# Optimization experiments

Measured on AMD Instinct MI355X. Metric: run time of the kernel, lower is better.

Reference implementation:

```python
import jax, jax.numpy as jnp
import numpy as np
import math

DIM = 1024
NUM_HEADS = 16


def setup_inputs() -> dict:
    key = jax.random.key(0)
    ks = jax.random.split(key, 6)
    B, S, D = 2, 2048, DIM
    return {
        "q": jax.random.normal(ks[0], (B, S, D), dtype=jnp.float32),
        "k": jax.random.normal(ks[1], (B, S, D), dtype=jnp.float32),
        "v": jax.random.normal(ks[2], (B, S, D), dtype=jnp.float32),
        "wq": jax.random.normal(ks[3], (D, D), dtype=jnp.float32),
        "wk": jax.random.normal(ks[4], (D, D), dtype=jnp.float32),
        "wv": jax.random.normal(ks[5], (D, D), dtype=jnp.float32),
    }


def reference(q, k, v, wq, wk, wv):
    B, S, D = q.shape
    H = NUM_HEADS
    hd = D // H
    # projections: [B,S,D] @ [D,D]
    qp = (q @ wq).reshape(B, H, S, hd)  # NOTE: direct reshape, as in the original
    kp = (k @ wk).reshape(B, H, S, hd)
    vp = (v @ wv).reshape(B, H, S, hd)
    scale = 1.0 / math.sqrt(D)  # original scales by sqrt(dim), not sqrt(head_dim)
    att = jnp.einsum("bhqd,bhkd->bhqk", qp, kp) * scale  # [B,H,S,S]
    att = jax.nn.softmax(att, axis=-1)
    out = jnp.einsum("bhqk,bhkd->bhqd", att, vp)  # [B,H,S,hd]
    out = out.transpose(0, 2, 1, 3).reshape(B, S, D)
    return out
```

## Files before the change

### kernel.cpp

```cpp
#include <hip/hip_runtime.h>
#include <hip/hip_bf16.h>
#include <stdint.h>

#define DIMD 1024
#define SEQ  2048
#define NH   16
#define MROWS 4096
#define NQ   65536

typedef __bf16 bf16_t;
typedef bf16_t bf16x8 __attribute__((ext_vector_type(8)));
typedef float  f32x4  __attribute__((ext_vector_type(4)));
typedef unsigned short u16;
typedef unsigned short u16x4 __attribute__((ext_vector_type(4)));
typedef unsigned short u16x8 __attribute__((ext_vector_type(8)));
typedef unsigned int   u32;
typedef u32 u32x2 __attribute__((ext_vector_type(2)));

static __device__ __forceinline__ f32x4 mfma16(bf16x8 a, bf16x8 b, f32x4 c) {
    return __builtin_amdgcn_mfma_f32_16x16x32_bf16(a, b, c, 0, 0, 0);
}

static __device__ __forceinline__ float fast_exp2(float x) {
#if __has_builtin(__builtin_amdgcn_exp2f)
    return __builtin_amdgcn_exp2f(x);
#else
    return exp2f(x);
#endif
}

#define GLD16(gsrc, ldst) __builtin_amdgcn_global_load_lds(                    \
    (const __attribute__((address_space(1))) unsigned int*)(gsrc),             \
    (__attribute__((address_space(3))) unsigned int*)(ldst), 16, 0, 0)

static __device__ __forceinline__ void split_bf16(float x, u16& h, u16& l) {
    u32 u = __float_as_uint(x);
    u16 hu = (u16)(u >> 16);
    float xh = __uint_as_float((u32)hu << 16);
    float lo = x - xh;
    h = hu;
    l = (u16)(__float_as_uint(lo) >> 16);
}

static __device__ __forceinline__ u32 pack_bf16(float a, float b) {
    return (__float_as_uint(a) >> 16) | (__float_as_uint(b) & 0xffff0000u);
}
static __device__ __forceinline__ u32 pack_bf16_rn(float a, float b) {
    u32 ua = __float_as_uint(a) + 0x8000u;
    u32 ub = __float_as_uint(b) + 0x8000u;
    return (ua >> 16) | (ub & 0xffff0000u);
}
static __device__ __forceinline__ float bf_to_f(u16 v) {
    return __uint_as_float((u32)v << 16);
}

__global__ __launch_bounds__(256) void transWs3(
    const float* __restrict__ w0, const float* __restrict__ w1, const float* __restrict__ w2,
    u16* __restrict__ WTsH, u16* __restrict__ WTsL) {
    const int z = blockIdx.z;
    const float* W = z == 0 ? w0 : z == 1 ? w1 : w2;
    __shared__ u16 Hs[4096], Ls[4096];
    const int tid = threadIdx.x;
    const int kt = blockIdx.x, nt = blockIdx.y;
    const int n0 = nt * 128, k0 = kt * 32;
    #pragma unroll
    for (int i = 0; i < 4; i++) {
        int f = i * 256 + tid;
        int kr = f >> 5, nc4 = (f & 31) * 4;
        f32x4 w = *(const f32x4*)&W[(size_t)(k0 + kr) * DIMD + n0 + nc4];
        int cc = kr >> 3, e = kr & 7;
        #pragma unroll
        for (int j = 0; j < 4; j++) {
            u16 hh, ll; split_bf16(w[j], hh, ll);
            Hs[cc * 1024 + (nc4 + j) * 8 + e] = hh;
            Ls[cc * 1024 + (nc4 + j) * 8 + e] = ll;
        }
    }
    __syncthreads();
    const size_t base = (size_t)z * (DIMD * DIMD) + (size_t)(nt * 32 + kt) * 4096;
    #pragma unroll
    for (int i = 0; i < 2; i++) {
        int idx = (i * 256 + tid) * 8;
        *(u16x8*)(WTsH + base + idx) = *(const u16x8*)&Hs[idx];
        *(u16x8*)(WTsL + base + idx) = *(const u16x8*)&Ls[idx];
    }
}

__global__ __launch_bounds__(256, 3) void proj7(
    const float* __restrict__ xq, const float* __restrict__ xk, const float* __restrict__ xv,
    const u16* __restrict__ WTsH, const u16* __restrict__ WTsL,
    u16* __restrict__ qh, u16* __restrict__ ql,
    u16* __restrict__ kh, u16* __restrict__ kl,
    u16* __restrict__ vh) {

    const int z = blockIdx.z;
    const float* X = z == 0 ? xq : z == 1 ? xk : xv;
    const u16* BH = WTsH + (size_t)z * (DIMD * DIMD);
    const u16* BL = WTsL + (size_t)z * (DIMD * DIMD);
    u16* outH = z == 0 ? qh : z == 1 ? kh : vh;
    u16* outL = z == 0 ? ql : kl;
    const float oscale = z == 0 ? 0.0450842200278f : 1.0f;

    __shared__ u16 lds[24576];
    u16* AsH = lds;
    u16* AsL = lds + 4096;

    const int tid  = threadIdx.x;
    const int lane = tid & 63, wave = tid >> 6;
    const int quad = lane >> 4, l16 = lane & 15;
    const int wy = wave >> 1, wx = wave & 1;
    const int m0 = blockIdx.x * 128;
    const int n0 = blockIdx.y * 128;
    const size_t Bregion0 = (size_t)(blockIdx.y * 32) * 4096;

    const int rA  = tid >> 2, ccA = tid & 3;
    const int idxA0 = ccA * 1024 + ((rA ^ (ccA << 1)) * 8);
    const int idxA1 = idxA0 + 512;
    const float* Xb0 = X + (size_t)(m0 + rA) * DIMD + ccA * 8;
    const float* Xb1 = X + (size_t)(m0 + rA + 64) * DIMD + ccA * 8;

    f32x4 acc[4][4];
    #pragma unroll
    for (int mt = 0; mt < 4; mt++)
        #pragma unroll
        for (int nt = 0; nt < 4; nt++) acc[mt][nt] = (f32x4)0.0f;

    f32x4 pa0, pa1, pa2, pa3;

#define LOADA(kt) do {                                                         \
        pa0 = *(const f32x4*)(Xb0 + (kt) * 32);                                \
        pa1 = *(const f32x4*)(Xb0 + (kt) * 32 + 4);                            \
        pa2 = *(const f32x4*)(Xb1 + (kt) * 32);                                \
        pa3 = *(const f32x4*)(Xb1 + (kt) * 32 + 4);                            \
    } while (0)

#define WRITEA() do {                                                          \
        u16x8 h, l;                                                            \
        _Pragma("unroll")                                                      \
        for (int j = 0; j < 4; j++) {                                          \
            u16 hh, ll;                                                        \
            split_bf16(pa0[j], hh, ll); h[j] = hh;     l[j] = ll;              \
            split_bf16(pa1[j], hh, ll); h[4 + j] = hh; l[4 + j] = ll;          \
        }                                                                      \
        *(u16x8*)&AsH[idxA0] = h;                                              \
        *(u16x8*)&AsL[idxA0] = l;                                              \
        _Pragma("unroll")                                                      \
        for (int j = 0; j < 4; j++) {                                          \
            u16 hh, ll;                                                        \
            split_bf16(pa2[j], hh, ll); h[j] = hh;     l[j] = ll;              \
            split_bf16(pa3[j], hh, ll); h[4 + j] = hh; l[4 + j] = ll;          \
        }                                                                      \
        *(u16x8*)&AsH[idxA1] = h;                                              \
        *(u16x8*)&AsL[idxA1] = l;                                              \
    } while (0)

#define STAGEB(kt, buf) do {                                                   \
        const size_t rb = Bregion0 + (size_t)(kt) * 4096;                      \
        u16* BsHd = lds + 8192 + (buf) * 8192;                                 \
        u16* BsLd = BsHd + 4096;                                               \
        int c0 = tid, c1 = 256 + tid;                                          \
        GLD16(BH + rb + c0 * 8, &BsHd[c0 * 8]);                                \
        GLD16(BH + rb + c1 * 8, &BsHd[c1 * 8]);                                \
        GLD16(BL + rb + c0 * 8, &BsLd[c0 * 8]);                                \
        GLD16(BL + rb + c1 * 8, &BsLd[c1 * 8]);                                \
    } while (0)

    LOADA(0);
    STAGEB(0, 0);
    WRITEA();
    __syncthreads();

    for (int kt = 0; kt < 32; kt++) {
        const int cur = kt & 1;
        if (kt < 31) {
            LOADA(kt + 1);
            STAGEB(kt + 1, cur ^ 1);
        }

        const u16* BsH = lds + 8192 + cur * 8192;
        const u16* BsL = BsH + 4096;

        bf16x8 aH[4], aL[4], bH[4], bL[4];
        #pragma unroll
        for (int mt = 0; mt < 4; mt++) {
            int r = wy * 64 + mt * 16 + l16;
            int idx = quad * 1024 + ((r ^ (quad << 1)) * 8);
            aH[mt] = *(const bf16x8*)&AsH[idx];
            aL[mt] = *(const bf16x8*)&AsL[idx];
        }
        #pragma unroll
        for (int nt = 0; nt < 4; nt++) {
            int r = wx * 64 + nt * 16 + l16;
            bH[nt] = *(const bf16x8*)&BsH[(quad * 128 + r) * 8];
            bL[nt] = *(const bf16x8*)&BsL[(quad * 128 + r) * 8];
        }
        #pragma unroll
        for (int mt = 0; mt < 4; mt++)
            #pragma unroll
            for (int nt = 0; nt < 4; nt++) {
                acc[mt][nt] = mfma16(aH[mt], bH[nt], acc[mt][nt]);
                acc[mt][nt] = mfma16(aH[mt], bL[nt], acc[mt][nt]);
                acc[mt][nt] = mfma16(aL[mt], bH[nt], acc[mt][nt]);
            }

        __syncthreads();
        if (kt < 31) WRITEA();
        __syncthreads();
    }
#undef LOADA
#undef WRITEA
#undef STAGEB

    #pragma unroll
    for (int mt = 0; mt < 4; mt++)
        #pragma unroll
        for (int nt = 0; nt < 4; nt++)
            #pragma unroll
            for (int r = 0; r < 4; r++) {
                int row = m0 + wy * 64 + mt * 16 + quad * 4 + r;
                int col = n0 + wx * 64 + nt * 16 + l16;
                u16 hh, ll; split_bf16(acc[mt][nt][r] * oscale, hh, ll);
                outH[(size_t)row * DIMD + col] = hh;
                if (z != 2) outL[(size_t)row * DIMD + col] = ll;
            }
}

__global__ __launch_bounds__(256) void transposeV(
    const u16* __restrict__ vh, u16* __restrict__ vt) {
    __shared__ u16 Ls[64][72];
    const int tid = threadIdx.x;
    const int bh = blockIdx.y;
    const int s0 = blockIdx.x * 64;
    const size_t slab = (size_t)bh * (SEQ * 64);
    #pragma unroll
    for (int i = 0; i < 2; i++) {
        int f = i * 256 + tid;
        int r = f >> 3, c = (f & 7) * 8;
        *(u16x8*)&Ls[r][c] = *(const u16x8*)(vh + slab + (size_t)(s0 + r) * 64 + c);
    }
    __syncthreads();
    #pragma unroll
    for (int i = 0; i < 2; i++) {
        int f = i * 256 + tid;
        int d = f >> 3, j = (f & 7) * 8;
        u16x8 o;
        #pragma unroll
        for (int jj = 0; jj < 8; jj++) o[jj] = Ls[j + jj][d];
        *(u16x8*)(vt + slab + (size_t)d * SEQ + s0 + j) = o;
    }
}

__global__ __launch_bounds__(512, 4) void flash8(
    const u16* __restrict__ qh, const u16* __restrict__ ql,
    const u16* __restrict__ kh, const u16* __restrict__ kl,
    const u16* __restrict__ vt,
    u16* __restrict__ Opart, float* __restrict__ Mpart, float* __restrict__ Lpart) {

    __shared__ u16 KH[64][72], KL[64][72], VTs[64][72];
    __shared__ u16 Ps[8][32][72];

    const int tid  = threadIdx.x;
    const int lane = tid & 63, wv = tid >> 6;
    const int quad = lane >> 4, l16 = lane & 15;
    const int bh = blockIdx.x, z = blockIdx.z;
    const size_t slab = (size_t)bh * (SEQ * 64);
    const int q0 = blockIdx.y * 256 + wv * 32;
    const int jbase = z * 1024;

    bf16x8 qfH[2][2], qfL[2][2];
    #pragma unroll
    for (int mq = 0; mq < 2; mq++) {
        const size_t rb = slab + (size_t)(q0 + mq * 16 + l16) * 64;
        #pragma unroll
        for (int kk = 0; kk < 2; kk++) {
            qfH[mq][kk] = *(const bf16x8*)(qh + rb + kk * 32 + quad * 8);
            qfL[mq][kk] = *(const bf16x8*)(ql + rb + kk * 32 + quad * 8);
        }
    }

    f32x4 O[2][4];
    float M[2] = {-3.0e38f, -3.0e38f}, L[2] = {0.0f, 0.0f};
    #pragma unroll
    for (int mq = 0; mq < 2; mq++)
        #pragma unroll
        for (int nv = 0; nv < 4; nv++) O[mq][nv] = (f32x4)0.0f;

    const int r0 = tid >> 3, c0 = (tid & 7) * 8;
    u16x8 s0, s2, s4;

    {
        const int j0 = jbase;
        s0 = *(const u16x8*)(kh + slab + (size_t)(j0 + r0) * 64 + c0);
        s2 = *(const u16x8*)(kl + slab + (size_t)(j0 + r0) * 64 + c0);
        s4 = *(const u16x8*)(vt + slab + (size_t)r0 * SEQ + j0 + c0);
    }
    *(u16x8*)&KH[r0][c0] = s0;
    *(u16x8*)&KL[r0][c0] = s2;
    *(u16x8*)&VTs[r0][c0] = s4;
    __syncthreads();

    for (int t = 0; t < 16; t++) {
        if (t < 15) {
            const int j0 = jbase + (t + 1) * 64;
            s0 = *(const u16x8*)(kh + slab + (size_t)(j0 + r0) * 64 + c0);
            s2 = *(const u16x8*)(kl + slab + (size_t)(j0 + r0) * 64 + c0);
            s4 = *(const u16x8*)(vt + slab + (size_t)r0 * SEQ + j0 + c0);
        }

        f32x4 St[2][4];
        #pragma unroll
        for (int mq = 0; mq < 2; mq++)
            #pragma unroll
            for (int nt = 0; nt < 4; nt++) St[mq][nt] = (f32x4)0.0f;
        __builtin_amdgcn_s_setprio(1);
        #pragma unroll
        for (int nt = 0; nt < 4; nt++) {
            const int rB = nt * 16 + l16;
            #pragma unroll
            for (int kk = 0; kk < 2; kk++) {
                bf16x8 kHf = *(const bf16x8*)&KH[rB][kk * 32 + quad * 8];
                bf16x8 kLf = *(const bf16x8*)&KL[rB][kk * 32 + quad * 8];
                #pragma unroll
                for (int mq = 0; mq < 2; mq++) {
                    St[mq][nt] = mfma16(kHf, qfH[mq][kk], St[mq][nt]);
                    St[mq][nt] = mfma16(kLf, qfH[mq][kk], St[mq][nt]);
                    St[mq][nt] = mfma16(kHf, qfL[mq][kk], St[mq][nt]);
                }
            }
        }
        __builtin_amdgcn_s_setprio(0);

        #pragma unroll
        for (int mq = 0; mq < 2; mq++) {
            float mx = St[mq][0][0];
            #pragma unroll
            for (int nt = 0; nt < 4; nt++)
                #pragma unroll
                for (int r = 0; r < 4; r++) mx = fmaxf(mx, St[mq][nt][r]);
            mx = fmaxf(mx, __shfl_xor(mx, 16));
            mx = fmaxf(mx, __shfl_xor(mx, 32));
            float Mn = M[mq];
            if (__any(mx > Mn)) {
                Mn = fmaxf(Mn, mx);
                float al = fast_exp2(M[mq] - Mn);
                M[mq] = Mn;
                L[mq] *= al;
                #pragma unroll
                for (int nv = 0; nv < 4; nv++) O[mq][nv] *= al;
            }
            float rs = 0.0f;
            #pragma unroll
            for (int nt = 0; nt < 4; nt++)
                #pragma unroll
                for (int r = 0; r < 4; r++) {
                    float p = fast_exp2(St[mq][nt][r] - Mn);
                    St[mq][nt][r] = p;
                    rs += p;
                }
            rs += __shfl_xor(rs, 16);
            rs += __shfl_xor(rs, 32);
            L[mq] += rs;
            #pragma unroll
            for (int nt = 0; nt < 4; nt++) {
                u32x2 d;
                d[0] = pack_bf16(St[mq][nt][0], St[mq][nt][1]);
                d[1] = pack_bf16(St[mq][nt][2], St[mq][nt][3]);
                *(u32x2*)&Ps[wv][mq * 16 + l16][nt * 16 + quad * 4] = d;
            }
        }

        __builtin_amdgcn_s_setprio(1);
        #pragma unroll
        for (int kk = 0; kk < 2; kk++) {
            bf16x8 pB[2];
            #pragma unroll
            for (int mq = 0; mq < 2; mq++)
                pB[mq] = *(const bf16x8*)&Ps[wv][mq * 16 + l16][kk * 32 + quad * 8];
            #pragma unroll
            for (int nv = 0; nv < 4; nv++) {
                bf16x8 vF = *(const bf16x8*)&VTs[nv * 16 + l16][kk * 32 + quad * 8];
                #pragma unroll
                for (int mq = 0; mq < 2; mq++)
                    O[mq][nv] = mfma16(vF, pB[mq], O[mq][nv]);
            }
        }
        __builtin_amdgcn_s_setprio(0);

        __syncthreads();
        if (t < 15) {
            *(u16x8*)&KH[r0][c0] = s0;
            *(u16x8*)&KL[r0][c0] = s2;
            *(u16x8*)&VTs[r0][c0] = s4;
        }
        __syncthreads();
    }

    const int qgb = bh * SEQ + q0;
    #pragma unroll
    for (int mq = 0; mq < 2; mq++) {
        const int qg = qgb + mq * 16 + l16;
        #pragma unroll
        for (int nv = 0; nv < 4; nv++) {
            u32x2 d;
            d[0] = pack_bf16_rn(O[mq][nv][0], O[mq][nv][1]);
            d[1] = pack_bf16_rn(O[mq][nv][2], O[mq][nv][3]);
            *(u32x2*)(Opart + ((size_t)(z * NQ + qg)) * 64 + nv * 16 + quad * 4) = d;
        }
        if (quad == 0) {
            Mpart[z * NQ + qg] = M[mq];
            Lpart[z * NQ + qg] = L[mq];
        }
    }
}

__global__ __launch_bounds__(256) void combineK(
    const u16* __restrict__ Opart, const float* __restrict__ Mpart,
    const float* __restrict__ Lpart, float* __restrict__ out) {
    int idx = blockIdx.x * 256 + threadIdx.x;
    int qg = idx >> 4, c4 = (idx & 15) * 4;
    float M0 = Mpart[qg], M1 = Mpart[NQ + qg];
    float L0 = Lpart[qg], L1 = Lpart[NQ + qg];
    float Ms = fmaxf(M0, M1);
    float w0 = fast_exp2(M0 - Ms), w1 = fast_exp2(M1 - Ms);
    float inv = 1.0f / (w0 * L0 + w1 * L1);
    u16x4 a = *(const u16x4*)&Opart[(size_t)qg * 64 + c4];
    u16x4 b = *(const u16x4*)&Opart[((size_t)NQ + qg) * 64 + c4];
    f32x4 o;
    #pragma unroll
    for (int j = 0; j < 4; j++)
        o[j] = (w0 * bf_to_f(a[j]) + w1 * bf_to_f(b[j])) * inv;
    int bh = qg >> 11, s = qg & 2047;
    int bb = bh >> 4, h = bh & 15;
    *(f32x4*)&out[((size_t)(bb * SEQ + s)) * DIMD + h * 64 + c4] = o;
}

extern "C" void kernel_launch(void* const* d_in, const int* in_sizes, int n_in,
                              void* d_out, int out_size, void* d_ws, size_t ws_size,
                              hipStream_t stream) {
    const float* q  = (const float*)d_in[0];
    const float* k  = (const float*)d_in[1];
    const float* v  = (const float*)d_in[2];
    const float* wq = (const float*)d_in[3];
    const float* wk = (const float*)d_in[4];
    const float* wv = (const float*)d_in[5];
    float* out = (float*)d_out;

    char* ws = (char*)d_ws;
    const size_t MB = 1 << 20;
    u16* qh   = (u16*)(ws + 0 * MB);
    u16* ql   = (u16*)(ws + 8 * MB);
    u16* kh   = (u16*)(ws + 16 * MB);
    u16* kl   = (u16*)(ws + 24 * MB);
    u16* vh   = (u16*)(ws + 32 * MB);
    u16* vt   = (u16*)(ws + 40 * MB);
    u16* WTsH = (u16*)(ws + 48 * MB);
    u16* WTsL = (u16*)(ws + 54 * MB);
    u16*   Opart = (u16*)(ws + 48 * MB);
    float* Mpart = (float*)(ws + 64 * MB);
    float* Lpart = (float*)(ws + 64 * MB + 512 * 1024);

    transWs3<<<dim3(32, 8, 3), 256, 0, stream>>>(wq, wk, wv, WTsH, WTsL);

    proj7<<<dim3(32, 8, 3), 256, 0, stream>>>(
        q, k, v, WTsH, WTsL, qh, ql, kh, kl, vh);

    transposeV<<<dim3(SEQ / 64, 2 * NH), 256, 0, stream>>>(vh, vt);

    flash8<<<dim3(2 * NH, SEQ / 256, 2), 512, 0, stream>>>(
        qh, ql, kh, kl, vt, Opart, Mpart, Lpart);

    combineK<<<dim3(NQ * 16 / 256), 256, 0, stream>>>(Opart, Mpart, Lpart, out);
}
```

Measured before the change: 276.7 us.

## Fuse V transpose into flash kernel via swizzled LDS staging, relax rescale threshold

Removes the separate transposeV kernel and its extra global round trip. The flash kernel now loads V rows directly and transposes them while storing into an XOR-swizzled shared-memory tile, using scalar 16-bit LDS writes. It also skips the online-softmax rescale unless the running max grows by more than 8 (log2 units), which cuts rescale work but lets exponentials grow up to 2^8 before renormalisation. The launch-bounds occupancy hint drops from 4 to 2 blocks.

```diff
diff --git a/kernel.cpp b/kernel.cpp
--- a/kernel.cpp
+++ b/kernel.cpp
@@ -225,35 +225,10 @@
             }
 }
 
-__global__ __launch_bounds__(256) void transposeV(
-    const u16* __restrict__ vh, u16* __restrict__ vt) {
-    __shared__ u16 Ls[64][72];
-    const int tid = threadIdx.x;
-    const int bh = blockIdx.y;
-    const int s0 = blockIdx.x * 64;
-    const size_t slab = (size_t)bh * (SEQ * 64);
-    #pragma unroll
-    for (int i = 0; i < 2; i++) {
-        int f = i * 256 + tid;
-        int r = f >> 3, c = (f & 7) * 8;
-        *(u16x8*)&Ls[r][c] = *(const u16x8*)(vh + slab + (size_t)(s0 + r) * 64 + c);
-    }
-    __syncthreads();
-    #pragma unroll
-    for (int i = 0; i < 2; i++) {
-        int f = i * 256 + tid;
-        int d = f >> 3, j = (f & 7) * 8;
-        u16x8 o;
-        #pragma unroll
-        for (int jj = 0; jj < 8; jj++) o[jj] = Ls[j + jj][d];
-        *(u16x8*)(vt + slab + (size_t)d * SEQ + s0 + j) = o;
-    }
-}
-
-__global__ __launch_bounds__(512, 4) void flash8(
+__global__ __launch_bounds__(512, 2) void flash13(
     const u16* __restrict__ qh, const u16* __restrict__ ql,
     const u16* __restrict__ kh, const u16* __restrict__ kl,
-    const u16* __restrict__ vt,
+    const u16* __restrict__ vh,
     u16* __restrict__ Opart, float* __restrict__ Mpart, float* __restrict__ Lpart) {
 
     __shared__ u16 KH[64][72], KL[64][72], VTs[64][72];
@@ -286,17 +261,24 @@
         for (int nv = 0; nv < 4; nv++) O[mq][nv] = (f32x4)0.0f;
 
     const int r0 = tid >> 3, c0 = (tid & 7) * 8;
+    const int vswz  = ((c0 >> 3) & 7) << 3;
+    const int vcol0 = r0 ^ vswz;
     u16x8 s0, s2, s4;
+
+#define STAGEV() do {                                                          \
+        _Pragma("unroll")                                                      \
+        for (int j = 0; j < 8; j++) VTs[c0 + j][vcol0] = (u16)s4[j];           \
+    } while (0)
 
     {
         const int j0 = jbase;
         s0 = *(const u16x8*)(kh + slab + (size_t)(j0 + r0) * 64 + c0);
         s2 = *(const u16x8*)(kl + slab + (size_t)(j0 + r0) * 64 + c0);
-        s4 = *(const u16x8*)(vt + slab + (size_t)r0 * SEQ + j0 + c0);
+        s4 = *(const u16x8*)(vh + slab + (size_t)(j0 + r0) * 64 + c0);
     }
     *(u16x8*)&KH[r0][c0] = s0;
     *(u16x8*)&KL[r0][c0] = s2;
-    *(u16x8*)&VTs[r0][c0] = s4;
+    STAGEV();
     __syncthreads();
 
     for (int t = 0; t < 16; t++) {
@@ -304,7 +286,7 @@
             const int j0 = jbase + (t + 1) * 64;
             s0 = *(const u16x8*)(kh + slab + (size_t)(j0 + r0) * 64 + c0);
             s2 = *(const u16x8*)(kl + slab + (size_t)(j0 + r0) * 64 + c0);
-            s4 = *(const u16x8*)(vt + slab + (size_t)r0 * SEQ + j0 + c0);
+            s4 = *(const u16x8*)(vh + slab + (size_t)(j0 + r0) * 64 + c0);
         }
 
         f32x4 St[2][4];
@@ -340,7 +322,7 @@
             mx = fmaxf(mx, __shfl_xor(mx, 16));
             mx = fmaxf(mx, __shfl_xor(mx, 32));
             float Mn = M[mq];
-            if (__any(mx > Mn)) {
+            if (__any(mx > Mn + 8.0f)) {
                 Mn = fmaxf(Mn, mx);
                 float al = fast_exp2(M[mq] - Mn);
                 M[mq] = Mn;
@@ -378,7 +360,9 @@
                 pB[mq] = *(const bf16x8*)&Ps[wv][mq * 16 + l16][kk * 32 + quad * 8];
             #pragma unroll
             for (int nv = 0; nv < 4; nv++) {
-                bf16x8 vF = *(const bf16x8*)&VTs[nv * 16 + l16][kk * 32 + quad * 8];
+                const int rowd = nv * 16 + l16;
+                const int colr = (kk * 32 + quad * 8) ^ (((rowd >> 3) & 7) << 3);
+                bf16x8 vF = *(const bf16x8*)&VTs[rowd][colr];
                 #pragma unroll
                 for (int mq = 0; mq < 2; mq++)
                     O[mq][nv] = mfma16(vF, pB[mq], O[mq][nv]);
@@ -390,10 +374,11 @@
         if (t < 15) {
             *(u16x8*)&KH[r0][c0] = s0;
             *(u16x8*)&KL[r0][c0] = s2;
-            *(u16x8*)&VTs[r0][c0] = s4;
+            STAGEV();
         }
         __syncthreads();
     }
+#undef STAGEV
 
     const int qgb = bh * SEQ + q0;
     #pragma unroll
@@ -452,22 +437,19 @@
     u16* kh   = (u16*)(ws + 16 * MB);
     u16* kl   = (u16*)(ws + 24 * MB);
     u16* vh   = (u16*)(ws + 32 * MB);
-    u16* vt   = (u16*)(ws + 40 * MB);
-    u16* WTsH = (u16*)(ws + 48 * MB);
-    u16* WTsL = (u16*)(ws + 54 * MB);
-    u16*   Opart = (u16*)(ws + 48 * MB);
-    float* Mpart = (float*)(ws + 64 * MB);
-    float* Lpart = (float*)(ws + 64 * MB + 512 * 1024);
+    u16* WTsH = (u16*)(ws + 40 * MB);
+    u16* WTsL = (u16*)(ws + 46 * MB);
+    u16* Opart = (u16*)(ws + 40 * MB);
+    float* Mpart = (float*)(ws + 56 * MB);
+    float* Lpart = (float*)(ws + 56 * MB + 512 * 1024);
 
     transWs3<<<dim3(32, 8, 3), 256, 0, stream>>>(wq, wk, wv, WTsH, WTsL);
 
     proj7<<<dim3(32, 8, 3), 256, 0, stream>>>(
         q, k, v, WTsH, WTsL, qh, ql, kh, kl, vh);
 
-    transposeV<<<dim3(SEQ / 64, 2 * NH), 256, 0, stream>>>(vh, vt);
-
-    flash8<<<dim3(2 * NH, SEQ / 256, 2), 512, 0, stream>>>(
-        qh, ql, kh, kl, vt, Opart, Mpart, Lpart);
+    flash13<<<dim3(2 * NH, SEQ / 256, 2), 512, 0, stream>>>(
+        qh, ql, kh, kl, vh, Opart, Mpart, Lpart);
 
     combineK<<<dim3(NQ * 16 / 256), 256, 0, stream>>>(Opart, Mpart, Lpart, out);
 }
```

Result: faster. 264.1 us (-4.6%).
